# Optimization experiments

Measured on AMD Instinct MI355X. Metric: run time of the kernel, lower is better.

Reference implementation:

```python
import jax, jax.numpy as jnp
import numpy as np

B, S, D_IN = 1, 2048, 2048
H, KV, HD = 32, 8, 64          # num_heads, num_kv_groups, head_dim
GS = H // KV                    # group_size
D_OUT = H * HD
EPS = 1e-6


def _rmsnorm(x, w):
    # RMSNormQwen over last dim (head_dim)
    var = jnp.mean(x * x, axis=-1, keepdims=True)
    return x * jax.lax.rsqrt(var + EPS) * w


def _rope(x, cos, sin):
    # rotate-half RoPE; x: [B, heads, S, HD], cos/sin: [S, HD]
    d = x.shape[-1]
    x1, x2 = x[..., : d // 2], x[..., d // 2 :]
    rot = jnp.concatenate([-x2, x1], axis=-1)
    return x * cos + rot * sin


def setup_inputs() -> dict:
    key = jax.random.key(0)
    ks = jax.random.split(key, 8)
    x = jax.random.normal(ks[0], (B, S, D_IN), dtype=jnp.float32)
    Wq = jax.random.normal(ks[1], (D_IN, D_OUT), dtype=jnp.float32) * 0.02
    Wk = jax.random.normal(ks[2], (D_IN, KV * HD), dtype=jnp.float32) * 0.02
    Wv = jax.random.normal(ks[3], (D_IN, KV * HD), dtype=jnp.float32) * 0.02
    Wo = jax.random.normal(ks[4], (D_OUT, D_IN), dtype=jnp.float32) * 0.02
    q_norm_w = jnp.ones((HD,), dtype=jnp.float32)
    k_norm_w = jnp.ones((HD,), dtype=jnp.float32)
    # causal mask: True where masked (j > i)
    mask = jnp.triu(jnp.ones((S, S), dtype=bool), k=1)
    # RoPE tables
    inv_freq = 1.0 / (10000.0 ** (np.arange(0, HD, 2, dtype=np.float32) / HD))
    ang = np.arange(S, dtype=np.float32)[:, None] * inv_freq[None, :]  # [S, HD/2]
    cos = jnp.asarray(np.concatenate([np.cos(ang), np.cos(ang)], axis=-1))
    sin = jnp.asarray(np.concatenate([np.sin(ang), np.sin(ang)], axis=-1))
    return {"x": x, "mask": mask, "cos": cos, "sin": sin,
            "Wq": Wq, "Wk": Wk, "Wv": Wv, "Wo": Wo,
            "q_norm_w": q_norm_w, "k_norm_w": k_norm_w}


def reference(x, mask, cos, sin, Wq, Wk, Wv, Wo, q_norm_w, k_norm_w):
    b, s, _ = x.shape
    q = (x @ Wq).reshape(b, s, H, HD).transpose(0, 2, 1, 3)   # [B,H,S,HD]
    k = (x @ Wk).reshape(b, s, KV, HD).transpose(0, 2, 1, 3)  # [B,KV,S,HD]
    v = (x @ Wv).reshape(b, s, KV, HD).transpose(0, 2, 1, 3)  # [B,KV,S,HD]
    q = _rmsnorm(q, q_norm_w)
    k = _rmsnorm(k, k_norm_w)
    q = _rope(q, cos, sin)
    k = _rope(k, cos, sin)
    # grouped-KV attention without materializing repeated K/V
    qg = q.reshape(b, KV, GS, s, HD)
    scores = jnp.einsum('bkgsd,bktd->bkgst', qg, k)           # [B,KV,GS,S,S]
    scores = jnp.where(mask, -jnp.inf, scores)
    weights = jax.nn.softmax(scores / (HD ** 0.5), axis=-1)
    ctx = jnp.einsum('bkgst,bktd->bkgsd', weights, v)         # [B,KV,GS,S,HD]
    ctx = ctx.reshape(b, H, s, HD).transpose(0, 2, 1, 3).reshape(b, s, D_OUT)
    return ctx @ Wo
```

## Files before the change

### kernel.cpp

```cpp
#include <hip/hip_runtime.h>
#include <hip/hip_bf16.h>
#include <math.h>

#define S_LEN 2048
#define DIN   2048
#define NH    32
#define NKV   8
#define HD    64
#define DOUT  2048
#define QKVN  3072
#define KOFF  2048
#define VOFF  2560

typedef __attribute__((ext_vector_type(8))) short short8v;
typedef __attribute__((ext_vector_type(8))) unsigned short ushort8v;
typedef __attribute__((ext_vector_type(4))) unsigned short ushort4v;
typedef __attribute__((ext_vector_type(4))) float float4v;
typedef __attribute__((ext_vector_type(16))) float float16v;

__device__ __forceinline__ float bf2f(unsigned short u) {
    union { float f; unsigned u; } c; c.u = ((unsigned)u) << 16; return c.f;
}
__device__ __forceinline__ unsigned short f2bf(float f) {
    union { float f; unsigned u; } c; c.f = f;
    unsigned r = c.u + 0x7fffu + ((c.u >> 16) & 1u);
    return (unsigned short)(r >> 16);
}
__device__ __forceinline__ unsigned short f2h(float f) {
    union { _Float16 h; unsigned short u; } c; c.h = (_Float16)f; return c.u;
}
__device__ __forceinline__ float h2f(unsigned short u) {
    union { _Float16 h; unsigned short u; } c; c.u = u; return (float)c.h;
}
__device__ __forceinline__ unsigned cvtpk(float lo, float hi) {
    unsigned r;
    asm("v_cvt_pk_bf16_f32 %0, %1, %2" : "=v"(r) : "v"(lo), "v"(hi));
    return r;
}
__device__ __forceinline__ float fexp2(float x) {
    float r;
    asm("v_exp_f32 %0, %1" : "=v"(r) : "v"(x));
    return r;
}

__global__ __launch_bounds__(256) void prep(const float* __restrict__ Wq,
                                            const float* __restrict__ Wk,
                                            const float* __restrict__ Wv,
                                            const float* __restrict__ Wo,
                                            const float* __restrict__ x,
                                            unsigned short* __restrict__ W1,
                                            unsigned short* __restrict__ WoT,
                                            unsigned short* __restrict__ XB) {
    __shared__ float t[32][33];
    const int a = blockIdx.x;
    const int tx = threadIdx.x & 31, ty = threadIdx.x >> 5;
    if (a < 6144) {
        const int n0 = (a % 96) * 32, k0 = (a / 96) * 32;
        const float* src; int nn0, Nsrc;
        if (n0 < KOFF)      { src = Wq; nn0 = n0;        Nsrc = DOUT; }
        else if (n0 < VOFF) { src = Wk; nn0 = n0 - KOFF; Nsrc = 512; }
        else                { src = Wv; nn0 = n0 - VOFF; Nsrc = 512; }
#pragma unroll
        for (int j = ty; j < 32; j += 8)
            t[j][tx] = src[(size_t)(k0 + j) * Nsrc + nn0 + tx];
        __syncthreads();
#pragma unroll
        for (int j = ty; j < 32; j += 8)
            W1[(size_t)(n0 + j) * DIN + k0 + tx] = f2bf(t[tx][j]);
    } else if (a < 10240) {
        const int b = a - 6144;
        const int n0 = (b % 64) * 32, k0 = (b / 64) * 32;
#pragma unroll
        for (int j = ty; j < 32; j += 8)
            t[j][tx] = Wo[(size_t)(k0 + j) * DIN + n0 + tx];
        __syncthreads();
#pragma unroll
        for (int j = ty; j < 32; j += 8)
            WoT[(size_t)(n0 + j) * DOUT + k0 + tx] = f2bf(t[tx][j]);
    } else {
        const int i = (a - 10240) * 1024 + threadIdx.x * 4;
        float4 v = *(const float4*)(x + i);
        XB[i + 0] = f2bf(v.x); XB[i + 1] = f2bf(v.y);
        XB[i + 2] = f2bf(v.z); XB[i + 3] = f2bf(v.w);
    }
}

template <int FUSE>
__global__ __launch_bounds__(256) void gemm64(const unsigned short* __restrict__ A,
                                              const unsigned short* __restrict__ Bt,
                                              void* __restrict__ Cv, int M, int N, int K,
                                              const float* __restrict__ qnw,
                                              const float* __restrict__ knw,
                                              const float* __restrict__ cosb,
                                              const float* __restrict__ sinb) {
    __shared__ __attribute__((aligned(16))) unsigned short As[2 * 128 * 64];
    __shared__ __attribute__((aligned(16))) unsigned short Bs[2 * 64 * 64];
    const int tid = threadIdx.x, lane = tid & 63, w = tid >> 6;
    const int bm = blockIdx.y * 128, bn = blockIdx.x * 64;
    const int wm = w * 32;

    float4v acc[2][4];
#pragma unroll
    for (int i = 0; i < 2; i++)
#pragma unroll
        for (int j = 0; j < 4; j++) acc[i][j] = (float4v){0.f, 0.f, 0.f, 0.f};

    const int srow = lane >> 3;
    const int schk = (lane & 7) ^ srow;
    const unsigned short* Ag[4];
    const unsigned short* Bg[2];
#pragma unroll
    for (int g = 0; g < 4; g++)
        Ag[g] = A + (size_t)(bm + w * 32 + g * 8 + srow) * K + schk * 8;
#pragma unroll
    for (int g = 0; g < 2; g++)
        Bg[g] = Bt + (size_t)(bn + w * 16 + g * 8 + srow) * K + schk * 8;

    auto STAGE = [&](int t, int b) {
        const size_t ko = (size_t)t * 64;
        unsigned short* Ad = As + b * (128 * 64) + (w * 32) * 64;
        unsigned short* Bd = Bs + b * (64 * 64) + (w * 16) * 64;
#pragma unroll
        for (int g = 0; g < 4; g++)
            __builtin_amdgcn_global_load_lds(
                (const __attribute__((address_space(1))) void*)(Ag[g] + ko),
                (__attribute__((address_space(3))) void*)(Ad + g * 8 * 64), 16, 0, 0);
#pragma unroll
        for (int g = 0; g < 2; g++)
            __builtin_amdgcn_global_load_lds(
                (const __attribute__((address_space(1))) void*)(Bg[g] + ko),
                (__attribute__((address_space(3))) void*)(Bd + g * 8 * 64), 16, 0, 0);
    };

    const int frow = lane & 15, quad = lane >> 4, sw = frow & 7;
    const int NT = K >> 6;

    STAGE(0, 0);

    for (int t = 0; t < NT; t++) {
        const int c = t & 1;
        if (t + 1 < NT) {
            STAGE(t + 1, c ^ 1);
            asm volatile("s_waitcnt vmcnt(6)" ::: "memory");
        } else {
            asm volatile("s_waitcnt vmcnt(0)" ::: "memory");
        }
        __builtin_amdgcn_s_barrier();
        __builtin_amdgcn_sched_barrier(0);

        const unsigned short* Ab = As + c * (128 * 64);
        const unsigned short* Bb = Bs + c * (64 * 64);
        short8v af[2][2], bf[4][2];
#pragma unroll
        for (int fm = 0; fm < 2; fm++)
#pragma unroll
            for (int ks = 0; ks < 2; ks++)
                af[fm][ks] = *(const short8v*)(Ab + (wm + fm * 16 + frow) * 64 +
                                               (((ks * 4 + quad) ^ sw) * 8));
#pragma unroll
        for (int fn = 0; fn < 4; fn++)
#pragma unroll
            for (int ks = 0; ks < 2; ks++)
                bf[fn][ks] = *(const short8v*)(Bb + (fn * 16 + frow) * 64 +
                                               (((ks * 4 + quad) ^ sw) * 8));
        __builtin_amdgcn_s_setprio(1);
#pragma unroll
        for (int ks = 0; ks < 2; ks++)
#pragma unroll
            for (int fm = 0; fm < 2; fm++)
#pragma unroll
                for (int fn = 0; fn < 4; fn++)
                    acc[fm][fn] = __builtin_amdgcn_mfma_f32_16x16x32_bf16(
                        af[fm][ks], bf[fn][ks], acc[fm][fn], 0, 0, 0);
        __builtin_amdgcn_s_setprio(0);

        if (t + 1 < NT) {
            asm volatile("s_waitcnt lgkmcnt(0)" ::: "memory");
            __builtin_amdgcn_sched_barrier(0);
            __builtin_amdgcn_s_barrier();
        }
    }

    const int quad4 = lane >> 4, col16 = lane & 15;
    if constexpr (FUSE == 1) {
        unsigned short* C = (unsigned short*)Cv;
        const int head = bn >> 6;
        if (head < 40) {
            const float* nw = (head < 32) ? qnw : knw;
            float wv[4];
#pragma unroll
            for (int fn = 0; fn < 4; fn++) wv[fn] = nw[fn * 16 + col16];
#pragma unroll
            for (int fm = 0; fm < 2; fm++)
#pragma unroll
                for (int r = 0; r < 4; r++) {
                    float x0 = acc[fm][0][r], x1 = acc[fm][1][r];
                    float x2 = acc[fm][2][r], x3 = acc[fm][3][r];
                    float ss = x0 * x0 + x1 * x1 + x2 * x2 + x3 * x3;
                    ss += __shfl_xor(ss, 1); ss += __shfl_xor(ss, 2);
                    ss += __shfl_xor(ss, 4); ss += __shfl_xor(ss, 8);
                    const float inv = rsqrtf(ss * (1.0f / 64.0f) + 1e-6f);
                    float xn[4] = {x0 * inv * wv[0], x1 * inv * wv[1],
                                   x2 * inv * wv[2], x3 * inv * wv[3]};
                    const int row = bm + wm + fm * 16 + quad4 * 4 + r;
                    const float* cr = cosb + (size_t)row * HD;
                    const float* sr = sinb + (size_t)row * HD;
#pragma unroll
                    for (int fn = 0; fn < 4; fn++) {
                        const float rot = (fn < 2) ? -xn[fn + 2] : xn[fn - 2];
                        const float res = xn[fn] * cr[fn * 16 + col16] +
                                          rot * sr[fn * 16 + col16];
                        C[(size_t)row * N + bn + fn * 16 + col16] = f2bf(res);
                    }
                }
        } else {
#pragma unroll
            for (int fm = 0; fm < 2; fm++)
#pragma unroll
                for (int fn = 0; fn < 4; fn++)
#pragma unroll
                    for (int r = 0; r < 4; r++)
                        C[(size_t)(bm + wm + fm * 16 + quad4 * 4 + r) * N +
                          bn + fn * 16 + col16] = f2bf(acc[fm][fn][r]);
        }
    } else {
        float* C = (float*)Cv;
#pragma unroll
        for (int fm = 0; fm < 2; fm++)
#pragma unroll
            for (int fn = 0; fn < 4; fn++)
#pragma unroll
                for (int r = 0; r < 4; r++)
                    C[(size_t)(bm + wm + fm * 16 + quad4 * 4 + r) * N +
                      bn + fn * 16 + col16] = acc[fm][fn][r];
    }
}

#define KSTR 72

__global__ __launch_bounds__(256, 3) void flash_part(const unsigned short* __restrict__ qb,
                                                     const unsigned short* __restrict__ kb,
                                                     const unsigned short* __restrict__ vb,
                                                     unsigned short* __restrict__ OpW,
                                                     unsigned short* __restrict__ OpD,
                                                     float* __restrict__ Lp) {
    __shared__ __attribute__((aligned(16))) unsigned short Ks[2][64 * KSTR];
    __shared__ __attribute__((aligned(16))) unsigned short Vt[2][64 * KSTR];

    const int tid = threadIdx.x, lane = tid & 63, w = tid >> 6;
    const int sl = lane & 31, hi = lane >> 5, hi8 = hi * 8;
    const int bid = blockIdx.x;
    const int g = bid & 7;
    const int p = (bid >> 3) & 31;
    const int c = bid >> 8;
    const int h = g * 4 + w;

    const int co   = c ? (9 + (c - 1) * 8) : 0;
    const int clen = c ? 8 : 9;

    const int s0a = p * 32, s0b = (63 - p) * 32;
    const int nta = (s0a + 95) >> 6;
    int nA = nta - co;
    nA = nA < 0 ? 0 : (nA > clen ? clen : nA);

    const float C1 = 0.18033688011112042f;
    const float C2 = 12.262908856239697f;

    unsigned short* OhA = OpW + (size_t)c * 1024 * DOUT;
    float*          LhA = Lp + (size_t)c * 1024 * NH;
    unsigned short* OhB = (c < 3) ? (OpW + (size_t)(2 + c) * 1024 * DOUT) : OpD;
    float*          LhB = Lp + (size_t)(2 + c) * 1024 * NH;

    int seg = (c < 2) ? 0 : 1;
    int s0 = seg == 0 ? s0a : s0b;

    short8v qf[4];
#pragma unroll
    for (int ksq = 0; ksq < 4; ksq++)
        qf[ksq] = *(const short8v*)(qb + (size_t)(s0 + sl) * QKVN + h * HD +
                                    ksq * 16 + hi8);

    float16v O[2], Lacc;
#pragma unroll
    for (int df = 0; df < 2; df++)
#pragma unroll
        for (int r = 0; r < 16; r++) O[df][r] = 0.f;
#pragma unroll
    for (int r = 0; r < 16; r++) Lacc[r] = 0.f;

    short8v ones;
#pragma unroll
    for (int i = 0; i < 8; i++) ones[i] = (short)0x3F80;

    const int kkey = tid >> 2, kch = tid & 3;
    const unsigned short* kg = kb + (size_t)kkey * QKVN + g * HD + kch * 16;
    const int kp = tid & 31, vdbb = tid >> 5;
    const unsigned short* vg0 = vb + (size_t)(2 * kp) * QKVN + g * HD + vdbb * 8;
    const unsigned short* vg1 = vg0 + QKVN;

    auto epi = [&](int sbase, unsigned short* Os, float* Ls, int roff) {
#pragma unroll
        for (int df = 0; df < 2; df++)
#pragma unroll
            for (int r = 0; r < 16; r++) {
                const int row = sbase + (r & 3) + 8 * (r >> 2) + 4 * hi - roff;
                Os[(size_t)row * DOUT + h * HD + df * 32 + sl] = f2h(O[df][r]);
            }
        if (sl == 0) {
#pragma unroll
            for (int r = 0; r < 16; r++) {
                const int row = sbase + (r & 3) + 8 * (r >> 2) + 4 * hi - roff;
                Ls[(size_t)row * NH + h] = Lacc[r];
            }
        }
    };
    auto zacc = [&]() {
#pragma unroll
        for (int df = 0; df < 2; df++)
#pragma unroll
            for (int r = 0; r < 16; r++) O[df][r] = 0.f;
#pragma unroll
        for (int r = 0; r < 16; r++) Lacc[r] = 0.f;
    };

    auto kt = [&](int jj) {
        const int sj = co + jj;
        return (sj < nta) ? sj : (sj - nta);
    };

    ushort8v ka0, ka1, va0, va1;
    auto LOADREGS = [&](int it) {
        const size_t off = (size_t)it * 64 * QKVN;
        ka0 = *(const ushort8v*)(kg + off);
        ka1 = *(const ushort8v*)(kg + off + 8);
        va0 = *(const ushort8v*)(vg0 + off);
        va1 = *(const ushort8v*)(vg1 + off);
    };
    auto COMMIT = [&](int b) {
        unsigned short* kd = Ks[b] + kkey * KSTR + kch * 16;
        *(ushort8v*)kd = ka0;
        *(ushort8v*)(kd + 8) = ka1;
        union { ushort8v v; unsigned d[4]; } ua, ub;
        ua.v = va0; ub.v = va1;
        unsigned short* vd = Vt[b] + (size_t)(vdbb * 8) * KSTR + 2 * kp;
#pragma unroll
        for (int i = 0; i < 8; i++) {
            const unsigned sel = (i & 1) ? 0x07060302u : 0x05040100u;
            const unsigned word = __builtin_amdgcn_perm(ub.d[i >> 1], ua.d[i >> 1], sel);
            *(unsigned*)(vd + (size_t)i * KSTR) = word;
        }
    };

    LOADREGS(kt(0));
    COMMIT(0);
    LOADREGS(kt(1));

#pragma unroll 1
    for (int jj = 0; jj < clen; jj++) {
        const int cur = jj & 1;
        __syncthreads();
        if (jj + 1 < clen) COMMIT(cur ^ 1);
        if (jj + 2 < clen) LOADREGS(kt(jj + 2));
        if (seg == 0 && jj == nA) {
            if (nA) {
                epi(s0a, OhA, LhA, 0);
                zacc();
            }
            s0 = s0b; seg = 1;
#pragma unroll
            for (int ksq = 0; ksq < 4; ksq++)
                qf[ksq] = *(const short8v*)(qb + (size_t)(s0b + sl) * QKVN +
                                            h * HD + ksq * 16 + hi8);
        }

        const int t0 = kt(jj) * 64;
        const bool edge = (t0 + 63 > s0);

#pragma unroll
        for (int b = 0; b < 2; b++) {
            short8v kf[4];
#pragma unroll
            for (int ksq = 0; ksq < 4; ksq++)
                kf[ksq] = *(const short8v*)(Ks[cur] + (32 * b + sl) * KSTR +
                                            ksq * 16 + hi8);
            float16v sct;
#pragma unroll
            for (int r = 0; r < 16; r++) sct[r] = 0.f;
            __builtin_amdgcn_s_setprio(1);
#pragma unroll
            for (int ksq = 0; ksq < 4; ksq++)
                sct = __builtin_amdgcn_mfma_f32_32x32x16_bf16(kf[ksq], qf[ksq],
                                                              sct, 0, 0, 0);
            __builtin_amdgcn_s_setprio(0);
#pragma unroll
            for (int r = 0; r < 16; r++) {
                float arg = sct[r] * C1 - C2;
                if (edge) {
                    const int kglob = t0 + 32 * b + (r & 3) + 8 * (r >> 2) + 4 * hi;
                    arg = (kglob <= s0 + sl) ? arg : -100.f;
                }
                sct[r] = fexp2(arg);
            }
            unsigned pk[8];
#pragma unroll
            for (int i = 0; i < 8; i++) pk[i] = cvtpk(sct[2 * i], sct[2 * i + 1]);
#pragma unroll
            for (int kk = 0; kk < 2; kk++) {
                unsigned x0 = pk[4 * kk + 0], x1 = pk[4 * kk + 1];
                unsigned y0 = pk[4 * kk + 2], y1 = pk[4 * kk + 3];
                asm("v_permlane32_swap_b32 %0, %1" : "+v"(x0), "+v"(y0));
                asm("v_permlane32_swap_b32 %0, %1" : "+v"(x1), "+v"(y1));
                union { unsigned u[4]; short8v v; } pa;
                pa.u[0] = x0; pa.u[1] = x1; pa.u[2] = y0; pa.u[3] = y1;
                const int ks = 2 * b + kk;
                __builtin_amdgcn_s_setprio(1);
#pragma unroll
                for (int df = 0; df < 2; df++) {
                    const short8v vf = *(const short8v*)(Vt[cur] +
                                                         (size_t)(df * 32 + sl) * KSTR +
                                                         ks * 16 + hi8);
                    O[df] = __builtin_amdgcn_mfma_f32_32x32x16_bf16(pa.v, vf,
                                                                    O[df], 0, 0, 0);
                }
                Lacc = __builtin_amdgcn_mfma_f32_32x32x16_bf16(pa.v, ones,
                                                               Lacc, 0, 0, 0);
                __builtin_amdgcn_s_setprio(0);
            }
        }
    }

    if (seg == 0) {
        epi(s0a, OhA, LhA, 0);
    } else {
        epi(s0b, OhB, LhB, 1024);
    }
}

__global__ __launch_bounds__(256) void combine(const unsigned short* __restrict__ OpW,
                                               const unsigned short* __restrict__ OpD,
                                               const float* __restrict__ Lp,
                                               unsigned short* __restrict__ CTX) {
    const int i4 = (blockIdx.x * 256 + threadIdx.x) * 4;
    const int row = i4 >> 11, hh = (i4 & 2047) >> 6;
    float acc[4];
    float l;
    if (row < 1024) {
        ushort4v a0 = *(const ushort4v*)(OpW + i4);
#pragma unroll
        for (int j = 0; j < 4; j++) acc[j] = h2f(a0[j]);
        l = Lp[(size_t)row * NH + hh];
        if (row >= 576) {
            ushort4v a1 = *(const ushort4v*)(OpW + (size_t)1024 * DOUT + i4);
#pragma unroll
            for (int j = 0; j < 4; j++) acc[j] += h2f(a1[j]);
            l += Lp[(size_t)(1024 + row) * NH + hh];
        }
    } else {
        const size_t j4 = (size_t)(row - 1024) * DOUT + (i4 & 2047);
        ushort4v b1 = *(const ushort4v*)(OpW + (size_t)3 * 1024 * DOUT + j4);
        ushort4v b2 = *(const ushort4v*)(OpW + (size_t)4 * 1024 * DOUT + j4);
        ushort4v b3 = *(const ushort4v*)(OpD + j4);
#pragma unroll
        for (int j = 0; j < 4; j++)
            acc[j] = h2f(b1[j]) + h2f(b2[j]) + h2f(b3[j]);
        const size_t lr = (size_t)(row - 1024) * NH + hh;
        l = Lp[(size_t)3 * 1024 * NH + lr] + Lp[(size_t)4 * 1024 * NH + lr] +
            Lp[(size_t)5 * 1024 * NH + lr];
        if (row >= 1536) {
            ushort4v b0 = *(const ushort4v*)(OpW + (size_t)2 * 1024 * DOUT + j4);
#pragma unroll
            for (int j = 0; j < 4; j++) acc[j] += h2f(b0[j]);
            l += Lp[(size_t)2 * 1024 * NH + lr];
        }
    }
    const float inv = 1.0f / l;
    ushort4v r;
#pragma unroll
    for (int j = 0; j < 4; j++) r[j] = f2bf(acc[j] * inv);
    *(ushort4v*)(CTX + i4) = r;
}

extern "C" void kernel_launch(void* const* d_in, const int* in_sizes, int n_in,
                              void* d_out, int out_size, void* d_ws, size_t ws_size,
                              hipStream_t stream) {
    const float* x    = (const float*)d_in[0];
    const float* cosb = (const float*)d_in[2];
    const float* sinb = (const float*)d_in[3];
    const float* Wq   = (const float*)d_in[4];
    const float* Wk   = (const float*)d_in[5];
    const float* Wv   = (const float*)d_in[6];
    const float* Wo   = (const float*)d_in[7];
    const float* qw   = (const float*)d_in[8];
    const float* kw   = (const float*)d_in[9];
    float* out = (float*)d_out;

    unsigned short* W1  = (unsigned short*)d_ws;
    unsigned short* XB  = W1 + (size_t)QKVN * DIN;
    unsigned short* WoT = XB + (size_t)S_LEN * DIN;
    unsigned short* QKV = WoT + (size_t)DIN * DOUT;
    unsigned short* OpW = (unsigned short*)d_ws;
    unsigned short* OpD = (unsigned short*)d_out;
    float*          Lp  = (float*)(OpD + (size_t)1024 * DOUT);
    unsigned short* CTX = QKV;

    dim3 blk256(256);

    prep<<<dim3(14336), blk256, 0, stream>>>(Wq, Wk, Wv, Wo, x, W1, WoT, XB);

    gemm64<1><<<dim3(QKVN / 64, S_LEN / 128), blk256, 0, stream>>>(
        XB, W1, QKV, S_LEN, QKVN, DIN, qw, kw, cosb, sinb);

    flash_part<<<dim3(NKV * 32 * 4), blk256, 0, stream>>>(
        QKV, QKV + KOFF, QKV + VOFF, OpW, OpD, Lp);

    combine<<<dim3(S_LEN * DOUT / 1024), blk256, 0, stream>>>(OpW, OpD, Lp, CTX);

    gemm64<0><<<dim3(DIN / 64, S_LEN / 128), blk256, 0, stream>>>(
        CTX, WoT, out, S_LEN, DIN, DOUT, nullptr, nullptr, nullptr, nullptr);
}
```

Baseline: 243.2 us.

## Replace MFMA row-sum with VALU accumulation, compact partial buffers, raise flash occupancy

The softmax denominator is now accumulated as a per-lane scalar sum of the exponentials plus a cross-half shuffle, replacing the extra MFMA against a ones vector. This frees the 16-float accumulator. The launch bound minimum rises from 3 to 4 blocks per CU to exploit the lower register use. Partial outputs are repacked into compact workspace slots sized to the rows actually produced, so the output buffer now only holds the L partials. Risks are register spilling at the higher occupancy and extra VALU adds in the inner loop.

Result: faster. 234.1 us (-3.7%).

```diff
diff --git a/kernel.cpp b/kernel.cpp
--- a/kernel.cpp
+++ b/kernel.cpp
@@ -42,6 +42,14 @@
     asm("v_exp_f32 %0, %1" : "=v"(r) : "v"(x));
     return r;
 }
+
+#define A0OFF ((size_t)0)
+#define A1OFF ((size_t)1024 * 2048)
+#define B0OFF (A1OFF + (size_t)448 * 2048)
+#define B1OFF (B0OFF + (size_t)512 * 2048)
+#define B2OFF (B1OFF + (size_t)1024 * 2048)
+#define B3OFF (B2OFF + (size_t)1024 * 2048)
+#define LSLOT ((size_t)2048 * NH)
 
 __global__ __launch_bounds__(256) void prep(const float* __restrict__ Wq,
                                             const float* __restrict__ Wk,
@@ -238,11 +246,10 @@
 
 #define KSTR 72
 
-__global__ __launch_bounds__(256, 3) void flash_part(const unsigned short* __restrict__ qb,
+__global__ __launch_bounds__(256, 4) void flash_part(const unsigned short* __restrict__ qb,
                                                      const unsigned short* __restrict__ kb,
                                                      const unsigned short* __restrict__ vb,
                                                      unsigned short* __restrict__ OpW,
-                                                     unsigned short* __restrict__ OpD,
                                                      float* __restrict__ Lp) {
     __shared__ __attribute__((aligned(16))) unsigned short Ks[2][64 * KSTR];
     __shared__ __attribute__((aligned(16))) unsigned short Vt[2][64 * KSTR];
@@ -266,10 +273,12 @@
     const float C1 = 0.18033688011112042f;
     const float C2 = 12.262908856239697f;
 
-    unsigned short* OhA = OpW + (size_t)c * 1024 * DOUT;
-    float*          LhA = Lp + (size_t)c * 1024 * NH;
-    unsigned short* OhB = (c < 3) ? (OpW + (size_t)(2 + c) * 1024 * DOUT) : OpD;
-    float*          LhB = Lp + (size_t)(2 + c) * 1024 * NH;
+    const size_t aoff = (c == 0) ? A0OFF : A1OFF;
+    const int    aroff = (c == 0) ? 0 : 576;
+    const size_t boff = (c == 0) ? B0OFF : (c == 1) ? B1OFF : (c == 2) ? B2OFF : B3OFF;
+    const int    broff = (c == 0) ? 1536 : 1024;
+    float* LhA = Lp + (size_t)c * LSLOT;
+    float* LhB = Lp + (size_t)(2 + c) * LSLOT;
 
     int seg = (c < 2) ? 0 : 1;
     int s0 = seg == 0 ? s0a : s0b;
@@ -280,17 +289,12 @@
         qf[ksq] = *(const short8v*)(qb + (size_t)(s0 + sl) * QKVN + h * HD +
                                     ksq * 16 + hi8);
 
-    float16v O[2], Lacc;
+    float16v O[2];
 #pragma unroll
     for (int df = 0; df < 2; df++)
 #pragma unroll
         for (int r = 0; r < 16; r++) O[df][r] = 0.f;
-#pragma unroll
-    for (int r = 0; r < 16; r++) Lacc[r] = 0.f;
-
-    short8v ones;
-#pragma unroll
-    for (int i = 0; i < 8; i++) ones[i] = (short)0x3F80;
+    float lsum = 0.f;
 
     const int kkey = tid >> 2, kch = tid & 3;
     const unsigned short* kg = kb + (size_t)kkey * QKVN + g * HD + kch * 16;
@@ -306,21 +310,15 @@
                 const int row = sbase + (r & 3) + 8 * (r >> 2) + 4 * hi - roff;
                 Os[(size_t)row * DOUT + h * HD + df * 32 + sl] = f2h(O[df][r]);
             }
-        if (sl == 0) {
-#pragma unroll
-            for (int r = 0; r < 16; r++) {
-                const int row = sbase + (r & 3) + 8 * (r >> 2) + 4 * hi - roff;
-                Ls[(size_t)row * NH + h] = Lacc[r];
-            }
-        }
+        float lt = lsum + __shfl_xor(lsum, 32);
+        if (hi == 0) Ls[(size_t)(sbase + sl) * NH + h] = lt;
     };
     auto zacc = [&]() {
 #pragma unroll
         for (int df = 0; df < 2; df++)
 #pragma unroll
             for (int r = 0; r < 16; r++) O[df][r] = 0.f;
-#pragma unroll
-        for (int r = 0; r < 16; r++) Lacc[r] = 0.f;
+        lsum = 0.f;
     };
 
     auto kt = [&](int jj) {
@@ -363,7 +361,7 @@
         if (jj + 2 < clen) LOADREGS(kt(jj + 2));
         if (seg == 0 && jj == nA) {
             if (nA) {
-                epi(s0a, OhA, LhA, 0);
+                epi(s0a, OpW + aoff, LhA, aroff);
                 zacc();
             }
             s0 = s0b; seg = 1;
@@ -399,7 +397,9 @@
                     const int kglob = t0 + 32 * b + (r & 3) + 8 * (r >> 2) + 4 * hi;
                     arg = (kglob <= s0 + sl) ? arg : -100.f;
                 }
-                sct[r] = fexp2(arg);
+                const float pv = fexp2(arg);
+                sct[r] = pv;
+                lsum += pv;
             }
             unsigned pk[8];
 #pragma unroll
@@ -422,55 +422,54 @@
                     O[df] = __builtin_amdgcn_mfma_f32_32x32x16_bf16(pa.v, vf,
                                                                     O[df], 0, 0, 0);
                 }
-                Lacc = __builtin_amdgcn_mfma_f32_32x32x16_bf16(pa.v, ones,
-                                                               Lacc, 0, 0, 0);
                 __builtin_amdgcn_s_setprio(0);
             }
         }
     }
 
     if (seg == 0) {
-        epi(s0a, OhA, LhA, 0);
+        epi(s0a, OpW + aoff, LhA, aroff);
     } else {
-        epi(s0b, OhB, LhB, 1024);
+        epi(s0b, OpW + boff, LhB, broff);
     }
 }
 
 __global__ __launch_bounds__(256) void combine(const unsigned short* __restrict__ OpW,
-                                               const unsigned short* __restrict__ OpD,
                                                const float* __restrict__ Lp,
                                                unsigned short* __restrict__ CTX) {
     const int i4 = (blockIdx.x * 256 + threadIdx.x) * 4;
     const int row = i4 >> 11, hh = (i4 & 2047) >> 6;
+    const int col = i4 & 2047;
     float acc[4];
     float l;
     if (row < 1024) {
-        ushort4v a0 = *(const ushort4v*)(OpW + i4);
+        ushort4v a0 = *(const ushort4v*)(OpW + A0OFF + (size_t)row * DOUT + col);
 #pragma unroll
         for (int j = 0; j < 4; j++) acc[j] = h2f(a0[j]);
         l = Lp[(size_t)row * NH + hh];
         if (row >= 576) {
-            ushort4v a1 = *(const ushort4v*)(OpW + (size_t)1024 * DOUT + i4);
+            ushort4v a1 = *(const ushort4v*)(OpW + A1OFF +
+                                             (size_t)(row - 576) * DOUT + col);
 #pragma unroll
             for (int j = 0; j < 4; j++) acc[j] += h2f(a1[j]);
-            l += Lp[(size_t)(1024 + row) * NH + hh];
+            l += Lp[LSLOT + (size_t)row * NH + hh];
         }
     } else {
-        const size_t j4 = (size_t)(row - 1024) * DOUT + (i4 & 2047);
-        ushort4v b1 = *(const ushort4v*)(OpW + (size_t)3 * 1024 * DOUT + j4);
-        ushort4v b2 = *(const ushort4v*)(OpW + (size_t)4 * 1024 * DOUT + j4);
-        ushort4v b3 = *(const ushort4v*)(OpD + j4);
+        const size_t j4 = (size_t)(row - 1024) * DOUT + col;
+        ushort4v b1 = *(const ushort4v*)(OpW + B1OFF + j4);
+        ushort4v b2 = *(const ushort4v*)(OpW + B2OFF + j4);
+        ushort4v b3 = *(const ushort4v*)(OpW + B3OFF + j4);
 #pragma unroll
         for (int j = 0; j < 4; j++)
             acc[j] = h2f(b1[j]) + h2f(b2[j]) + h2f(b3[j]);
-        const size_t lr = (size_t)(row - 1024) * NH + hh;
-        l = Lp[(size_t)3 * 1024 * NH + lr] + Lp[(size_t)4 * 1024 * NH + lr] +
-            Lp[(size_t)5 * 1024 * NH + lr];
+        const size_t lr = (size_t)row * NH + hh;
+        l = Lp[3 * LSLOT + lr] + Lp[4 * LSLOT + lr] + Lp[5 * LSLOT + lr];
         if (row >= 1536) {
-            ushort4v b0 = *(const ushort4v*)(OpW + (size_t)2 * 1024 * DOUT + j4);
+            ushort4v b0 = *(const ushort4v*)(OpW + B0OFF +
+                                             (size_t)(row - 1536) * DOUT + col);
 #pragma unroll
             for (int j = 0; j < 4; j++) acc[j] += h2f(b0[j]);
-            l += Lp[(size_t)2 * 1024 * NH + lr];
+            l += Lp[2 * LSLOT + lr];
         }
     }
     const float inv = 1.0f / l;
@@ -499,8 +498,7 @@
     unsigned short* WoT = XB + (size_t)S_LEN * DIN;
     unsigned short* QKV = WoT + (size_t)DIN * DOUT;
     unsigned short* OpW = (unsigned short*)d_ws;
-    unsigned short* OpD = (unsigned short*)d_out;
-    float*          Lp  = (float*)(OpD + (size_t)1024 * DOUT);
+    float*          Lp  = (float*)d_out;
     unsigned short* CTX = QKV;
 
     dim3 blk256(256);
@@ -511,9 +509,9 @@
         XB, W1, QKV, S_LEN, QKVN, DIN, qw, kw, cosb, sinb);
 
     flash_part<<<dim3(NKV * 32 * 4), blk256, 0, stream>>>(
-        QKV, QKV + KOFF, QKV + VOFF, OpW, OpD, Lp);
-
-    combine<<<dim3(S_LEN * DOUT / 1024), blk256, 0, stream>>>(OpW, OpD, Lp, CTX);
+        QKV, QKV + KOFF, QKV + VOFF, OpW, Lp);
+
+    combine<<<dim3(S_LEN * DOUT / 1024), blk256, 0, stream>>>(OpW, Lp, CTX);
 
     gemm64<0><<<dim3(DIN / 64, S_LEN / 128), blk256, 0, stream>>>(
         CTX, WoT, out, S_LEN, DIN, DOUT, nullptr, nullptr, nullptr, nullptr);
```
